# Kernel optimization log

Measured on AMD Instinct MI355X. Metric: run time of the kernel, lower is better.

## Reference

```python
import jax, jax.numpy as jnp
import numpy as np

B, N, C, H = 8, 1024, 512, 8
EPS = 1e-6


def setup_inputs() -> dict:
    key = jax.random.key(0)
    k0, k1, k2, k3, k4 = jax.random.split(key, 5)
    x = jax.random.normal(k0, (B, N, C), dtype=jnp.float32)
    # nonnegative random-walk visit-frequency mask stand-in
    mask = jax.random.uniform(k1, (N, N), dtype=jnp.float32)
    w_qkv = jax.random.normal(k2, (C, 3 * C), dtype=jnp.float32) * 0.02
    w_out = jax.random.normal(k3, (C, C), dtype=jnp.float32) * 0.02
    b_out = jax.random.normal(k4, (C,), dtype=jnp.float32) * 0.02
    return {"x": x, "mask": mask, "w_qkv": w_qkv, "w_out": w_out, "b_out": b_out}


def reference(x, mask, w_qkv, w_out, b_out):
    b, n, c = x.shape
    d = c // H
    qkv = x @ w_qkv                                   # [B,N,3C]
    q, k, v = jnp.split(qkv, 3, axis=-1)

    def to_heads(t):
        return t.reshape(b, n, H, d).transpose(0, 2, 1, 3)  # [B,H,N,D]

    q, k, v = to_heads(q), to_heads(k), to_heads(v)
    # positive feature map
    q = jax.nn.relu(q) + EPS
    k = jax.nn.relu(k) + EPS
    # graph diffusion: (q^T @ mask)^T == einsum over source node m
    q = q + 0.1 * jnp.einsum('bhmd,mn->bhnd', q, mask)
    k = k + 0.1 * jnp.einsum('bhmd,mn->bhnd', k, mask)
    # linear kernel scores, elementwise-masked
    kernel = jnp.einsum('bhnd,bhmd->bhnm', q, k) * mask   # [B,H,N,N]
    z = 1.0 / (kernel.sum(axis=-1, keepdims=True) + EPS)  # [B,H,N,1]
    out = jnp.einsum('bhnm,bhmd->bhnd', kernel, v) * z    # [B,H,N,D]
    out = out.transpose(0, 2, 1, 3).reshape(b, n, c)      # [B,N,C]
    return out @ w_out + b_out
```

## Files before the change

### kernel.cpp

```cpp
#include <hip/hip_runtime.h>
#include <cstddef>

#define Bsz 8
#define Nn  1024
#define Cc  512
#define Hh  8
#define Dd  64
#define EPSF 1e-6f

typedef __attribute__((ext_vector_type(8))) short short8;
typedef __attribute__((ext_vector_type(4))) float floatx4;

static __device__ __forceinline__ short f2bf(float f) {
    union { float f; unsigned u; } v; v.f = f;
    unsigned r = (v.u + 0x7FFFu + ((v.u >> 16) & 1u)) >> 16;
    return (short)r;
}
static __device__ __forceinline__ float bf2f(short s) {
    union { unsigned u; float f; } v; v.u = ((unsigned)(unsigned short)s) << 16;
    return v.f;
}

#define GLOAD_LDS16(gp, lp)                                              \
    __builtin_amdgcn_global_load_lds(                                    \
        (const __attribute__((address_space(1))) void*)(gp),             \
        (__attribute__((address_space(3))) void*)(lp), 16, 0, 0)

static __device__ __forceinline__
void stage_tile(short* __restrict__ lds, const short* __restrict__ src,
                int ldsrc, int tid, int CHUNKS, int SLOTS) {
    #pragma unroll
    for (int s = tid; s < SLOTS; s += 256) {
        int r = s / CHUNKS, cs = s % CHUNKS;
        int gc = cs ^ (r & 7);
        GLOAD_LDS16(&src[(size_t)r * ldsrc + gc * 8], &lds[s * 8]);
    }
}
static __device__ __forceinline__
short8 fragT(const short* __restrict__ lds, int CHUNKS, int r, int lc) {
    return *(const short8*)&lds[(r * CHUNKS + (lc ^ (r & 7))) * 8];
}

#define FENCE() asm volatile("" ::: "memory")
#define BARRIER_RAW() do { FENCE(); __builtin_amdgcn_s_barrier(); FENCE(); } while (0)
#define WAITVM(N) asm volatile("s_waitcnt vmcnt(" #N ")" ::: "memory")

__global__ __launch_bounds__(256)
void prep_all(const float* __restrict__ x, const float* __restrict__ mask,
              const float* __restrict__ wq, const float* __restrict__ wo,
              short* __restrict__ xb, short* __restrict__ Ad,
              short* __restrict__ wqT, short* __restrict__ woT,
              short* __restrict__ mbf) {
    __shared__ float t[64][65];
    const int tid = threadIdx.x;
    const int bid = blockIdx.x;

    if (bid < 2048) {
        int idx = bid * 256 + tid;
        const float* s = &x[(size_t)idx * 8];
        union { short h[8]; int4 v; } u;
        #pragma unroll
        for (int j = 0; j < 8; j++) u.h[j] = f2bf(s[j]);
        *(int4*)&xb[(size_t)idx * 8] = u.v;
        return;
    }
    if (bid < 2304) {
        int idx = bid - 2048;
        const int n0 = (idx & 15) * 64, m0 = (idx >> 4) * 64;
        #pragma unroll
        for (int i = 0; i < 4; i++) {
            int k = i * 256 + tid;
            int r = k >> 4, c4 = (k & 15) * 4;
            *(float4*)&t[r][c4] = *(const float4*)&mask[(size_t)(m0 + r) * Nn + n0 + c4];
        }
        __syncthreads();
        #pragma unroll
        for (int i = 0; i < 4; i++) {
            int k = i * 256 + tid;
            int rr = k >> 4, c4 = (k & 15) * 4;
            union { short h[4]; int2 v; } u;
            #pragma unroll
            for (int j = 0; j < 4; j++) {
                int mm = c4 + j;
                float v = 0.1f * t[mm][rr] + ((n0 + rr) == (m0 + mm) ? 1.0f : 0.0f);
                u.h[j] = f2bf(v);
            }
            *(int2*)&Ad[(size_t)(n0 + rr) * Nn + m0 + c4] = u.v;
        }
        return;
    }
    if (bid < 2496) {
        int idx = bid - 2304;
        const int n0 = (idx % 24) * 64, k0 = (idx / 24) * 64;
        #pragma unroll
        for (int i = 0; i < 4; i++) {
            int k = i * 256 + tid;
            int r = k >> 4, c4 = (k & 15) * 4;
            *(float4*)&t[r][c4] = *(const float4*)&wq[(size_t)(k0 + r) * 1536 + n0 + c4];
        }
        __syncthreads();
        #pragma unroll
        for (int i = 0; i < 4; i++) {
            int k = i * 256 + tid;
            int rr = k >> 4, c4 = (k & 15) * 4;
            union { short h[4]; int2 v; } u;
            #pragma unroll
            for (int j = 0; j < 4; j++) u.h[j] = f2bf(t[c4 + j][rr]);
            *(int2*)&wqT[(size_t)(n0 + rr) * 512 + k0 + c4] = u.v;
        }
        return;
    }
    if (bid < 2560) {
        int idx = bid - 2496;
        const int n0 = (idx & 7) * 64, k0 = (idx >> 3) * 64;
        #pragma unroll
        for (int i = 0; i < 4; i++) {
            int k = i * 256 + tid;
            int r = k >> 4, c4 = (k & 15) * 4;
            *(float4*)&t[r][c4] = *(const float4*)&wo[(size_t)(k0 + r) * 512 + n0 + c4];
        }
        __syncthreads();
        #pragma unroll
        for (int i = 0; i < 4; i++) {
            int k = i * 256 + tid;
            int rr = k >> 4, c4 = (k & 15) * 4;
            union { short h[4]; int2 v; } u;
            #pragma unroll
            for (int j = 0; j < 4; j++) u.h[j] = f2bf(t[c4 + j][rr]);
            *(int2*)&woT[(size_t)(n0 + rr) * 512 + k0 + c4] = u.v;
        }
        return;
    }
    {
        int idx = (bid - 2560) * 256 + tid;
        const float* s = &mask[(size_t)idx * 8];
        union { short h[8]; int4 v; } u;
        #pragma unroll
        for (int j = 0; j < 8; j++) u.h[j] = f2bf(s[j]);
        *(int4*)&mbf[(size_t)idx * 8] = u.v;
    }
}

static __device__ __forceinline__
void stageA_half(short* __restrict__ buf, const short* __restrict__ gA,
                 int kt, int h, int tid) {
    #pragma unroll
    for (int kk = 0; kk < 2; kk++) {
        int i = tid + kk * 512;
        int run = i >> 9;
        int within = i & 511;
        int r = run * 128 + h * 64 + (within >> 3);
        int c = within & 7;
        int gc = c ^ (r & 7);
        GLOAD_LDS16(gA + (size_t)r * 512 + kt + gc * 8, buf + (r * 8 + c) * 8);
    }
}
static __device__ __forceinline__
void stageB_half(short* __restrict__ buf, const short* __restrict__ gB,
                 int kt, int h, int tid) {
    #pragma unroll
    for (int kk = 0; kk < 2; kk++) {
        int i = tid + kk * 512;
        int run = i >> 8;
        int within = i & 255;
        int r = run * 64 + h * 32 + (within >> 3);
        int c = within & 7;
        int gc = c ^ (r & 7);
        GLOAD_LDS16(gB + (size_t)r * 512 + kt + gc * 8, buf + (r * 8 + c) * 8);
    }
}

template<int MH>
static __device__ __forceinline__
void readA8(const short* __restrict__ bufA, short8 (&aF)[4][2],
            int wr, int l16, int quad) {
    #pragma unroll
    for (int f = 0; f < 4; f++)
        #pragma unroll
        for (int kk = 0; kk < 2; kk++)
            aF[f][kk] = fragT(bufA, 8, wr * 128 + MH * 64 + f * 16 + l16, kk * 4 + quad);
}
template<int NH>
static __device__ __forceinline__
void readB4(const short* __restrict__ bufB, short8 (&bF)[2][2],
            int wc, int l16, int quad) {
    #pragma unroll
    for (int g = 0; g < 2; g++)
        #pragma unroll
        for (int kk = 0; kk < 2; kk++)
            bF[g][kk] = fragT(bufB, 8, wc * 64 + NH * 32 + g * 16 + l16, kk * 4 + quad);
}
template<int MH, int NH>
static __device__ __forceinline__
void mfma16(short8 (&aF)[4][2], short8 (&bF)[2][2], floatx4 (&acc)[8][4]) {
    #pragma unroll
    for (int kk = 0; kk < 2; kk++)
        #pragma unroll
        for (int f = 0; f < 4; f++)
            #pragma unroll
            for (int g = 0; g < 2; g++)
                acc[MH * 4 + f][NH * 2 + g] = __builtin_amdgcn_mfma_f32_16x16x32_bf16(
                    aF[f][kk], bF[g][kk], acc[MH * 4 + f][NH * 2 + g], 0, 0, 0);
}

__global__ __launch_bounds__(512, 2)
void gemm_qkv(const short* __restrict__ xb, const short* __restrict__ wqT,
              short* __restrict__ qT, short* __restrict__ kT,
              short* __restrict__ vT) {
    extern __shared__ short smem[];

    const int tid = threadIdx.x;
    const int lin = blockIdx.x;
    const int wgid = (lin & 7) * 24 + (lin >> 3);
    const int mt = wgid / 6, nt = wgid % 6;
    const int m0 = mt * 256, n0 = nt * 256;

    const int wid = tid >> 6, lane = tid & 63;
    const int quad = lane >> 4, l16 = lane & 15;
    const int wr = wid >> 2, wc = wid & 3;

    const short* Ab = xb  + (size_t)m0 * 512;
    const short* Bb = wqT + (size_t)n0 * 512;

    floatx4 acc[8][4];
    #pragma unroll
    for (int i = 0; i < 8; i++)
        #pragma unroll
        for (int j = 0; j < 4; j++) acc[i][j] = (floatx4){0.f, 0.f, 0.f, 0.f};

    short8 aF[4][2], bF[2][2];

    stageA_half(smem,          Ab, 0, 0, tid);
    stageB_half(smem + 16384,  Bb, 0, 0, tid);
    stageA_half(smem,          Ab, 0, 1, tid);
    stageB_half(smem + 16384,  Bb, 0, 1, tid);
    WAITVM(4); BARRIER_RAW();

    for (int j = 0; j < 8; ++j) {
        const short* cA = smem + (j & 1) * 32768;
        const short* cB = cA + 16384;
        short* nA = smem + ((j + 1) & 1) * 32768;
        short* nB = nA + 16384;
        const int kn = ((j + 1) & 7) * 64;

        readA8<0>(cA, aF, wr, l16, quad);
        readB4<0>(cB, bF, wc, l16, quad);
        stageA_half(nA, Ab, kn, 0, tid);
        stageB_half(nB, Bb, kn, 0, tid);
        BARRIER_RAW();
        __builtin_amdgcn_s_setprio(1);
        mfma16<0, 0>(aF, bF, acc);
        __builtin_amdgcn_s_setprio(0);
        WAITVM(4); BARRIER_RAW();

        readA8<1>(cA, aF, wr, l16, quad);
        stageA_half(nA, Ab, kn, 1, tid);
        stageB_half(nB, Bb, kn, 1, tid);
        BARRIER_RAW();
        __builtin_amdgcn_s_setprio(1);
        mfma16<1, 0>(aF, bF, acc);
        __builtin_amdgcn_s_setprio(0);
        BARRIER_RAW();

        readB4<1>(cB, bF, wc, l16, quad);
        BARRIER_RAW();
        __builtin_amdgcn_s_setprio(1);
        mfma16<1, 1>(aF, bF, acc);
        __builtin_amdgcn_s_setprio(0);
        BARRIER_RAW();

        readA8<0>(cA, aF, wr, l16, quad);
        BARRIER_RAW();
        __builtin_amdgcn_s_setprio(1);
        mfma16<0, 1>(aF, bF, acc);
        __builtin_amdgcn_s_setprio(0);
        WAITVM(4); BARRIER_RAW();
    }

    WAITVM(0); BARRIER_RAW();

    short* T = smem + wid * 8192;
    const int doRelu = (n0 < 1024);
    #pragma unroll
    for (int mf = 0; mf < 8; mf++)
        #pragma unroll
        for (int nf = 0; nf < 4; nf++)
            #pragma unroll
            for (int rr = 0; rr < 4; rr++) {
                float v = acc[mf][nf][rr];
                if (doRelu) v = fmaxf(v, 0.0f) + EPSF;
                int row = nf * 16 + l16;
                int col = mf * 16 + quad * 4 + rr;
                T[row * 128 + (col ^ ((row & 15) << 3))] = f2bf(v);
            }
    const int gm0 = m0 + wr * 128;
    const int b = gm0 >> 10, m_in0 = gm0 & 1023;
    #pragma unroll
    for (int g = 0; g < 4; g++) {
        int row = (lane >> 2) + g * 16;
        int gn = n0 + wc * 64 + row;
        int part = gn >> 9, ci = gn & 511;
        short* base = (part == 0) ? qT : (part == 1) ? kT : vT;
        short* dst = base + ((size_t)b * 512 + ci) * 1024 + m_in0;
        #pragma unroll
        for (int cc = 0; cc < 4; cc++) {
            int cs = ((lane & 3) + cc * 4) * 8;
            *(int4*)&dst[cs] = *(const int4*)&T[row * 128 + (cs ^ ((row & 15) << 3))];
        }
    }
}

__global__ __launch_bounds__(256)
void gemm_diff(const short* __restrict__ Ad, const short* __restrict__ qT,
               const short* __restrict__ kT, short* __restrict__ qd,
               short* __restrict__ kd) {
    __shared__ short smem[16384];
    short* As = smem;
    short* Bs = smem + 8192;

    const int tid = threadIdx.x;
    const int z = blockIdx.x, b = z >> 1, part = z & 1;
    const short* BTb = (part ? kT : qT) + (size_t)b * 512 * 1024;
    short* outb = (part ? kd : qd) + (size_t)b * 1024 * 512;

    const int c0 = blockIdx.y * 128;
    const int r0 = blockIdx.z * 128;
    const int wave = tid >> 6, lane = tid & 63;
    const int quad = lane >> 4, l16 = lane & 15;
    const int wm = (wave >> 1) * 64, wn = (wave & 1) * 64;

    floatx4 acc[4][4];
    #pragma unroll
    for (int i = 0; i < 4; i++)
        #pragma unroll
        for (int j = 0; j < 4; j++) acc[i][j] = (floatx4){0.f, 0.f, 0.f, 0.f};

    const short* Ab = Ad  + (size_t)r0 * 1024;
    const short* Bb = BTb + (size_t)c0 * 1024;

    for (int k0 = 0; k0 < 1024; k0 += 64) {
        __syncthreads();
        stage_tile(As, Ab + k0, 1024, tid, 8, 1024);
        stage_tile(Bs, Bb + k0, 1024, tid, 8, 1024);
        __syncthreads();
        #pragma unroll
        for (int kh = 0; kh < 2; kh++) {
            short8 a[4], b2[4];
            #pragma unroll
            for (int i = 0; i < 4; i++) a[i]  = fragT(As, 8, wm + i * 16 + l16, kh * 4 + quad);
            #pragma unroll
            for (int i = 0; i < 4; i++) b2[i] = fragT(Bs, 8, wn + i * 16 + l16, kh * 4 + quad);
            #pragma unroll
            for (int mi = 0; mi < 4; mi++)
                #pragma unroll
                for (int ni = 0; ni < 4; ni++)
                    acc[mi][ni] = __builtin_amdgcn_mfma_f32_16x16x32_bf16(
                        a[mi], b2[ni], acc[mi][ni], 0, 0, 0);
        }
    }

    #pragma unroll
    for (int mi = 0; mi < 4; mi++)
        #pragma unroll
        for (int r = 0; r < 4; r++) {
            int n = r0 + wm + mi * 16 + quad * 4 + r;
            #pragma unroll
            for (int ni = 0; ni < 4; ni++) {
                int c = c0 + wn + ni * 16 + l16;
                outb[(size_t)n * 512 + c] = f2bf(acc[mi][ni][r]);
            }
        }
}

__global__ __launch_bounds__(256)
void attn_mfma(const short* __restrict__ qd, const short* __restrict__ kd,
               const short* __restrict__ vTg, const short* __restrict__ mbf,
               short* __restrict__ abf) {
    __shared__ short qs[8192];
    __shared__ short ks[4096];
    __shared__ short vt[4096];
    __shared__ short ss[8192];
    __shared__ short ms[8192];

    const int tid = threadIdx.x;
    const int bh = blockIdx.x;
    const int b = bh >> 3, h = bh & 7;
    const int n0 = blockIdx.y * 128;

    const int wave = tid >> 6, lane = tid & 63;
    const int quad = lane >> 4, l16 = lane & 15;

    const short* Qb = qd + ((size_t)b * Nn + n0) * Cc + h * Dd;
    const short* Kb = kd + (size_t)b * Nn * Cc + h * Dd;
    const short* Vb = vTg + ((size_t)b * Cc + h * Dd) * Nn;
    const short* Mb = mbf + (size_t)n0 * Nn;

    stage_tile(qs, Qb, Cc, tid, 8, 1024);
    __syncthreads();
    short8 aT[2][2];
    #pragma unroll
    for (int t = 0; t < 2; t++) {
        aT[t][0] = fragT(qs, 8, wave * 32 + t * 16 + l16, quad);
        aT[t][1] = fragT(qs, 8, wave * 32 + t * 16 + l16, 4 + quad);
    }

    float dreg[2] = {0.f, 0.f};
    floatx4 nacc[2][4];
    #pragma unroll
    for (int t = 0; t < 2; t++)
        #pragma unroll
        for (int i = 0; i < 4; i++) nacc[t][i] = (floatx4){0.f, 0.f, 0.f, 0.f};

    const int ssrow[2] = { wave * 32 + l16, wave * 32 + 16 + l16 };

    for (int m0 = 0; m0 < Nn; m0 += 64) {
        __syncthreads();
        stage_tile(ks, Kb + (size_t)m0 * Cc, Cc, tid, 8, 512);
        stage_tile(vt, Vb + m0, Nn, tid, 8, 512);
        stage_tile(ms, Mb + m0, Nn, tid, 8, 1024);
        __syncthreads();

        #pragma unroll
        for (int mt = 0; mt < 4; mt++) {
            const short8 k0f = fragT(ks, 8, mt * 16 + l16, quad);
            const short8 k1f = fragT(ks, 8, mt * 16 + l16, 4 + quad);
            #pragma unroll
            for (int t = 0; t < 2; t++) {
                floatx4 s = (floatx4){0.f, 0.f, 0.f, 0.f};
                s = __builtin_amdgcn_mfma_f32_16x16x32_bf16(k0f, aT[t][0], s, 0, 0, 0);
                s = __builtin_amdgcn_mfma_f32_16x16x32_bf16(k1f, aT[t][1], s, 0, 0, 0);
                const int row = ssrow[t];
                const int c = mt * 16 + quad * 4;
                const int off = (row * 8 + ((c >> 3) ^ (row & 7))) * 8 + (c & 7);
                union { short h[4]; int2 v; } mk;
                mk.v = *(const int2*)&ms[off];
                float sv0 = s[0] * bf2f(mk.h[0]);
                float sv1 = s[1] * bf2f(mk.h[1]);
                float sv2 = s[2] * bf2f(mk.h[2]);
                float sv3 = s[3] * bf2f(mk.h[3]);
                dreg[t] += (sv0 + sv1) + (sv2 + sv3);
                union { short h[4]; int2 v; } pk;
                pk.h[0] = f2bf(sv0); pk.h[1] = f2bf(sv1);
                pk.h[2] = f2bf(sv2); pk.h[3] = f2bf(sv3);
                *(int2*)&ss[off] = pk.v;
            }
        }

        short8 p[2][2];
        #pragma unroll
        for (int t = 0; t < 2; t++) {
            p[t][0] = fragT(ss, 8, wave * 32 + t * 16 + l16, quad);
            p[t][1] = fragT(ss, 8, wave * 32 + t * 16 + l16, 4 + quad);
        }
        #pragma unroll
        for (int dt = 0; dt < 4; dt++) {
            const short8 v0 = fragT(vt, 8, dt * 16 + l16, quad);
            const short8 v1 = fragT(vt, 8, dt * 16 + l16, 4 + quad);
            #pragma unroll
            for (int t = 0; t < 2; t++) {
                nacc[t][dt] = __builtin_amdgcn_mfma_f32_16x16x32_bf16(p[t][0], v0, nacc[t][dt], 0, 0, 0);
                nacc[t][dt] = __builtin_amdgcn_mfma_f32_16x16x32_bf16(p[t][1], v1, nacc[t][dt], 0, 0, 0);
            }
        }
    }

    #pragma unroll
    for (int t = 0; t < 2; t++) {
        dreg[t] += __shfl_xor(dreg[t], 16, 64);
        dreg[t] += __shfl_xor(dreg[t], 32, 64);
    }

    #pragma unroll
    for (int t = 0; t < 2; t++)
        #pragma unroll
        for (int r = 0; r < 4; r++) {
            int nloc = quad * 4 + r;
            float den = __shfl(dreg[t], nloc, 64);
            int n = n0 + wave * 32 + t * 16 + nloc;
            float zr = 1.0f / (den + EPSF);
            #pragma unroll
            for (int dt = 0; dt < 4; dt++) {
                size_t o = ((size_t)b * Nn + n) * Cc + h * Dd + dt * 16 + l16;
                abf[o] = f2bf(nacc[t][dt][r] * zr);
            }
        }
}

__global__ __launch_bounds__(256)
void gemm_out(const short* __restrict__ abf, const short* __restrict__ woT,
              const float* __restrict__ bias, float* __restrict__ out) {
    __shared__ short smem[12288];
    short* As = smem;
    short* Bs = smem + 4096;

    const int tid = threadIdx.x;
    const int m0 = blockIdx.y * 64;
    const int n0 = blockIdx.x * 128;
    const int wave = tid >> 6, lane = tid & 63;
    const int quad = lane >> 4, l16 = lane & 15;
    const int wm = (wave >> 1) * 32, wn = (wave & 1) * 64;

    floatx4 acc[2][4];
    #pragma unroll
    for (int i = 0; i < 2; i++)
        #pragma unroll
        for (int j = 0; j < 4; j++) acc[i][j] = (floatx4){0.f, 0.f, 0.f, 0.f};

    const short* Ab = abf + (size_t)m0 * 512;
    const short* Bb = woT + (size_t)n0 * 512;

    for (int k0 = 0; k0 < 512; k0 += 64) {
        __syncthreads();
        stage_tile(As, Ab + k0, 512, tid, 8, 512);
        stage_tile(Bs, Bb + k0, 512, tid, 8, 1024);
        __syncthreads();
        #pragma unroll
        for (int kh = 0; kh < 2; kh++) {
            short8 a[2], b[4];
            #pragma unroll
            for (int i = 0; i < 2; i++)
                a[i] = fragT(As, 8, wm + i * 16 + l16, kh * 4 + quad);
            #pragma unroll
            for (int i = 0; i < 4; i++)
                b[i] = fragT(Bs, 8, wn + i * 16 + l16, kh * 4 + quad);
            #pragma unroll
            for (int mi = 0; mi < 2; mi++)
                #pragma unroll
                for (int ni = 0; ni < 4; ni++)
                    acc[mi][ni] = __builtin_amdgcn_mfma_f32_16x16x32_bf16(
                        a[mi], b[ni], acc[mi][ni], 0, 0, 0);
        }
    }

    #pragma unroll
    for (int mi = 0; mi < 2; mi++)
        #pragma unroll
        for (int r = 0; r < 4; r++) {
            int m = m0 + wm + mi * 16 + quad * 4 + r;
            #pragma unroll
            for (int ni = 0; ni < 4; ni++) {
                int n = n0 + wn + ni * 16 + l16;
                out[(size_t)m * 512 + n] = acc[mi][ni][r] + bias[n];
            }
        }
}

extern "C" void kernel_launch(void* const* d_in, const int* in_sizes, int n_in,
                              void* d_out, int out_size, void* d_ws, size_t ws_size,
                              hipStream_t stream) {
    const float* x     = (const float*)d_in[0];
    const float* mask  = (const float*)d_in[1];
    const float* w_qkv = (const float*)d_in[2];
    const float* w_out = (const float*)d_in[3];
    const float* b_out = (const float*)d_in[4];
    float* out = (float*)d_out;

    char* p = (char*)d_ws;
    short* xb  = (short*)p; p += 8388608;
    short* wqT = (short*)p; p += 1572864;
    short* Ad  = (short*)p; p += 2097152;
    short* woT = (short*)p; p += 524288;
    short* mbf = (short*)p; p += 2097152;
    short* qT  = (short*)p; p += 8388608;
    short* kT  = (short*)p; p += 8388608;
    short* vT  = (short*)p; p += 8388608;
    short* qd  = (short*)p; p += 8388608;
    short* kd  = (short*)p; p += 8388608;
    short* abf = (short*)p; p += 8388608;

    static int attr_set = 0;
    if (!attr_set) {
        hipFuncSetAttribute(reinterpret_cast<const void*>(gemm_qkv),
                            hipFuncAttributeMaxDynamicSharedMemorySize, 131072);
        attr_set = 1;
    }

    dim3 blk(256);

    prep_all  <<<3072, blk, 0, stream>>>(x, mask, w_qkv, w_out,
                                         xb, Ad, wqT, woT, mbf);
    gemm_qkv  <<<dim3(192), dim3(512), 131072, stream>>>(xb, wqT, qT, kT, vT);
    gemm_diff <<<dim3(16, 4, 8), blk, 0, stream>>>(Ad, qT, kT, qd, kd);
    attn_mfma <<<dim3(64, 8),  blk, 0, stream>>>(qd, kd, vT, mbf, abf);
    gemm_out  <<<dim3(4, 128), blk, 0, stream>>>(abf, woT, b_out, out);
}
```

Before: 165.9 us.

## Rewrite diffusion GEMM as double-buffered 8-wave pipelined kernel with larger tiles

Result: no change. 166.2 us (median of 2 runs) (+0.2%).

```diff
diff --git a/kernel.cpp b/kernel.cpp
--- a/kernel.cpp
+++ b/kernel.cpp
@@ -310,24 +310,82 @@
     }
 }
 
-__global__ __launch_bounds__(256)
-void gemm_diff(const short* __restrict__ Ad, const short* __restrict__ qT,
-               const short* __restrict__ kT, short* __restrict__ qd,
-               short* __restrict__ kd) {
-    __shared__ short smem[16384];
-    short* As = smem;
-    short* Bs = smem + 8192;
+static __device__ __forceinline__
+void dstageA_half(short* __restrict__ buf, const short* __restrict__ gA,
+                  int kt, int h, int tid) {
+    #pragma unroll
+    for (int kk = 0; kk < 2; kk++) {
+        int i = tid + kk * 512;
+        int rl = i >> 3;
+        int c  = i & 7;
+        int r  = (rl >> 5) * 64 + h * 32 + (rl & 31);
+        int gc = c ^ (r & 7);
+        GLOAD_LDS16(gA + (size_t)r * 1024 + kt + gc * 8, buf + (r * 8 + c) * 8);
+    }
+}
+static __device__ __forceinline__
+void dstageB_half(short* __restrict__ buf, const short* __restrict__ gB,
+                  int kt, int h, int tid) {
+    int rl = tid >> 3;
+    int c  = tid & 7;
+    int r  = (rl >> 5) * 64 + h * 32 + (rl & 31);
+    int gc = c ^ (r & 7);
+    GLOAD_LDS16(gB + (size_t)r * 1024 + kt + gc * 8, buf + (r * 8 + c) * 8);
+}
+template<int MH>
+static __device__ __forceinline__
+void dreadA(const short* __restrict__ bufA, short8 (&aF)[2][2],
+            int wr, int l16, int quad) {
+    #pragma unroll
+    for (int f = 0; f < 2; f++)
+        #pragma unroll
+        for (int kk = 0; kk < 2; kk++)
+            aF[f][kk] = fragT(bufA, 8, wr * 64 + MH * 32 + f * 16 + l16, kk * 4 + quad);
+}
+template<int NH>
+static __device__ __forceinline__
+void dreadB(const short* __restrict__ bufB, short8 (&bF)[2][2],
+            int wc, int l16, int quad) {
+    #pragma unroll
+    for (int g = 0; g < 2; g++)
+        #pragma unroll
+        for (int kk = 0; kk < 2; kk++)
+            bF[g][kk] = fragT(bufB, 8, wc * 64 + NH * 32 + g * 16 + l16, kk * 4 + quad);
+}
+template<int MH, int NH>
+static __device__ __forceinline__
+void dmfma8(short8 (&aF)[2][2], short8 (&bF)[2][2], floatx4 (&acc)[4][4]) {
+    #pragma unroll
+    for (int kk = 0; kk < 2; kk++)
+        #pragma unroll
+        for (int f = 0; f < 2; f++)
+            #pragma unroll
+            for (int g = 0; g < 2; g++)
+                acc[MH * 2 + f][NH * 2 + g] = __builtin_amdgcn_mfma_f32_16x16x32_bf16(
+                    aF[f][kk], bF[g][kk], acc[MH * 2 + f][NH * 2 + g], 0, 0, 0);
+}
+
+__global__ __launch_bounds__(512, 2)
+void gemm_diff8(const short* __restrict__ Ad, const short* __restrict__ qT,
+                const short* __restrict__ kT, short* __restrict__ qd,
+                short* __restrict__ kd) {
+    extern __shared__ short smem[];
 
     const int tid = threadIdx.x;
-    const int z = blockIdx.x, b = z >> 1, part = z & 1;
-    const short* BTb = (part ? kT : qT) + (size_t)b * 512 * 1024;
+    const int lin = blockIdx.x;
+    const int wgid = (lin & 7) * 32 + (lin >> 3);
+    const int mt = wgid >> 6, ct = wgid & 63;
+    const int m0 = mt * 256;
+    const int seg = ct >> 2, cb = (ct & 3) * 128;
+    const int b = seg >> 1, part = seg & 1;
+
+    const short* Bb = ((part ? kT : qT) + (size_t)b * 512 * 1024) + (size_t)cb * 1024;
     short* outb = (part ? kd : qd) + (size_t)b * 1024 * 512;
-
-    const int c0 = blockIdx.y * 128;
-    const int r0 = blockIdx.z * 128;
-    const int wave = tid >> 6, lane = tid & 63;
+    const short* Abase = Ad + (size_t)m0 * 1024;
+
+    const int wid = tid >> 6, lane = tid & 63;
     const int quad = lane >> 4, l16 = lane & 15;
-    const int wm = (wave >> 1) * 64, wn = (wave & 1) * 64;
+    const int wr = wid >> 1, wc = wid & 1;
 
     floatx4 acc[4][4];
     #pragma unroll
@@ -335,39 +393,65 @@
         #pragma unroll
         for (int j = 0; j < 4; j++) acc[i][j] = (floatx4){0.f, 0.f, 0.f, 0.f};
 
-    const short* Ab = Ad  + (size_t)r0 * 1024;
-    const short* Bb = BTb + (size_t)c0 * 1024;
-
-    for (int k0 = 0; k0 < 1024; k0 += 64) {
-        __syncthreads();
-        stage_tile(As, Ab + k0, 1024, tid, 8, 1024);
-        stage_tile(Bs, Bb + k0, 1024, tid, 8, 1024);
-        __syncthreads();
-        #pragma unroll
-        for (int kh = 0; kh < 2; kh++) {
-            short8 a[4], b2[4];
-            #pragma unroll
-            for (int i = 0; i < 4; i++) a[i]  = fragT(As, 8, wm + i * 16 + l16, kh * 4 + quad);
-            #pragma unroll
-            for (int i = 0; i < 4; i++) b2[i] = fragT(Bs, 8, wn + i * 16 + l16, kh * 4 + quad);
-            #pragma unroll
-            for (int mi = 0; mi < 4; mi++)
-                #pragma unroll
-                for (int ni = 0; ni < 4; ni++)
-                    acc[mi][ni] = __builtin_amdgcn_mfma_f32_16x16x32_bf16(
-                        a[mi], b2[ni], acc[mi][ni], 0, 0, 0);
-        }
-    }
-
-    #pragma unroll
-    for (int mi = 0; mi < 4; mi++)
-        #pragma unroll
-        for (int r = 0; r < 4; r++) {
-            int n = r0 + wm + mi * 16 + quad * 4 + r;
-            #pragma unroll
-            for (int ni = 0; ni < 4; ni++) {
-                int c = c0 + wn + ni * 16 + l16;
-                outb[(size_t)n * 512 + c] = f2bf(acc[mi][ni][r]);
+    short8 aF[2][2], bF[2][2];
+
+    dstageA_half(smem,          Abase, 0, 0, tid);
+    dstageB_half(smem + 16384,  Bb,    0, 0, tid);
+    dstageA_half(smem,          Abase, 0, 1, tid);
+    dstageB_half(smem + 16384,  Bb,    0, 1, tid);
+    WAITVM(3); BARRIER_RAW();
+
+    for (int j = 0; j < 16; ++j) {
+        const short* cA = smem + (j & 1) * 24576;
+        const short* cB = cA + 16384;
+        short* nA = smem + ((j + 1) & 1) * 24576;
+        short* nB = nA + 16384;
+        const int kn = ((j + 1) & 15) * 64;
+
+        dreadA<0>(cA, aF, wr, l16, quad);
+        dreadB<0>(cB, bF, wc, l16, quad);
+        dstageA_half(nA, Abase, kn, 0, tid);
+        dstageB_half(nB, Bb,    kn, 0, tid);
+        BARRIER_RAW();
+        __builtin_amdgcn_s_setprio(1);
+        dmfma8<0, 0>(aF, bF, acc);
+        __builtin_amdgcn_s_setprio(0);
+        WAITVM(3); BARRIER_RAW();
+
+        dreadA<1>(cA, aF, wr, l16, quad);
+        dstageA_half(nA, Abase, kn, 1, tid);
+        dstageB_half(nB, Bb,    kn, 1, tid);
+        BARRIER_RAW();
+        __builtin_amdgcn_s_setprio(1);
+        dmfma8<1, 0>(aF, bF, acc);
+        __builtin_amdgcn_s_setprio(0);
+        BARRIER_RAW();
+
+        dreadB<1>(cB, bF, wc, l16, quad);
+        BARRIER_RAW();
+        __builtin_amdgcn_s_setprio(1);
+        dmfma8<1, 1>(aF, bF, acc);
+        __builtin_amdgcn_s_setprio(0);
+        BARRIER_RAW();
+
+        dreadA<0>(cA, aF, wr, l16, quad);
+        BARRIER_RAW();
+        __builtin_amdgcn_s_setprio(1);
+        dmfma8<0, 1>(aF, bF, acc);
+        __builtin_amdgcn_s_setprio(0);
+        WAITVM(3); BARRIER_RAW();
+    }
+    WAITVM(0);
+
+    #pragma unroll
+    for (int fr = 0; fr < 4; fr++)
+        #pragma unroll
+        for (int rr = 0; rr < 4; rr++) {
+            int n = m0 + wr * 64 + fr * 16 + quad * 4 + rr;
+            #pragma unroll
+            for (int fc = 0; fc < 4; fc++) {
+                int c = cb + wc * 64 + fc * 16 + l16;
+                outb[(size_t)n * 512 + c] = f2bf(acc[fr][fc][rr]);
             }
         }
 }
@@ -572,6 +656,8 @@
     if (!attr_set) {
         hipFuncSetAttribute(reinterpret_cast<const void*>(gemm_qkv),
                             hipFuncAttributeMaxDynamicSharedMemorySize, 131072);
+        hipFuncSetAttribute(reinterpret_cast<const void*>(gemm_diff8),
+                            hipFuncAttributeMaxDynamicSharedMemorySize, 98304);
         attr_set = 1;
     }
 
@@ -580,7 +666,7 @@
     prep_all  <<<3072, blk, 0, stream>>>(x, mask, w_qkv, w_out,
                                          xb, Ad, wqT, woT, mbf);
     gemm_qkv  <<<dim3(192), dim3(512), 131072, stream>>>(xb, wqT, qT, kT, vT);
-    gemm_diff <<<dim3(16, 4, 8), blk, 0, stream>>>(Ad, qT, kT, qd, kd);
+    gemm_diff8<<<dim3(256), dim3(512), 98304, stream>>>(Ad, qT, kT, qd, kd);
     attn_mfma <<<dim3(64, 8),  blk, 0, stream>>>(qd, kd, vT, mbf, abf);
     gemm_out  <<<dim3(4, 128), blk, 0, stream>>>(abf, woT, b_out, out);
 }
```
